# Optimization experiments

Hardware: AMD Instinct MI355X
Metric: run time of the kernel (lower is better)

## Reference

```python
import jax, jax.numpy as jnp
import numpy as np

EPSILON = 1e-13
LN_EPS = 1e-5
DIRECTIONS = 2
HID = 512


def setup_inputs() -> dict:
    key = jax.random.key(0)
    k1, k2, k3, k4 = jax.random.split(key, 4)
    B, N, D = 16, 1024, HID
    adj = jax.random.randint(k1, (B, N, N), 0, 3, dtype=jnp.int32)  # labels 0..2
    hid = jax.random.normal(k2, (B, N, D), dtype=jnp.float32)
    W = jax.random.normal(k3, (DIRECTIONS * D, D), dtype=jnp.float32) * (1.0 / np.sqrt(DIRECTIONS * D))
    b = jnp.zeros((D,), dtype=jnp.float32)
    gamma = jnp.ones((D,), dtype=jnp.float32)
    beta = jnp.zeros((D,), dtype=jnp.float32)
    return {"adj": adj, "hid": hid, "W": W, "b": b, "gamma": gamma, "beta": beta}


def _layer_norm(x, gamma, beta):
    mu = jnp.mean(x, axis=-1, keepdims=True)
    var = jnp.mean(jnp.square(x - mu), axis=-1, keepdims=True)
    return (x - mu) * jax.lax.rsqrt(var + LN_EPS) * gamma + beta


def reference(adj, hid, W, b, gamma, beta):
    residual = hid
    direct_list = []
    for j in range(DIRECTIONS):  # fixed small structural loop
        mask = (adj == (j + 1)).astype(hid.dtype)            # [B,N,N]
        weight = mask / (jnp.sum(mask, axis=-1, keepdims=True) + EPSILON)
        direct_list.append(jnp.einsum('bnm,bmd->bnd', weight, hid))
    out = jnp.concatenate(direct_list, axis=-1)              # [B,N,directions*D]
    out = out @ W + b                                        # [B,N,D]
    out = jax.nn.relu(out)
    out = out + residual
    return _layer_norm(out, gamma, beta)
```

## Files before the change

### kernel.cpp

```cpp
#include <hip/hip_runtime.h>

#define NB 16
#define NN 1024
#define ND 512

typedef __attribute__((ext_vector_type(8))) short short8;
typedef __attribute__((ext_vector_type(4))) float f32x4;

typedef const __attribute__((address_space(1))) void* gptr1;
typedef __attribute__((address_space(3))) void* lptr3;

#define VMCNT0() asm volatile("s_waitcnt vmcnt(0)" ::: "memory")
#define VMCNT1() asm volatile("s_waitcnt vmcnt(1)" ::: "memory")
#define LGKM0()  asm volatile("s_waitcnt lgkmcnt(0)" ::: "memory")
#define BAR()    __builtin_amdgcn_s_barrier()

static __device__ __forceinline__ unsigned f2bf(float f) {
  union { float f; unsigned u; } v; v.f = f;
  unsigned r = v.u + 0x7FFFu + ((v.u >> 16) & 1u);
  return r >> 16;
}

__global__ void k_wt(const float* __restrict__ W, unsigned short* __restrict__ WT) {
  __shared__ float t[64][65];
  int r0 = blockIdx.x * 64;
  int c0 = blockIdx.y * 64;
  int tid = threadIdx.x;
#pragma unroll
  for (int i = 0; i < 4; ++i) {
    int f = i * 256 + tid;
    int r = f >> 4, cq = f & 15;
    float4 v = *(const float4*)(W + (size_t)(r0 + r) * ND + c0 + cq * 4);
    t[r][cq * 4 + 0] = v.x; t[r][cq * 4 + 1] = v.y;
    t[r][cq * 4 + 2] = v.z; t[r][cq * 4 + 3] = v.w;
  }
  __syncthreads();
#pragma unroll
  for (int i = 0; i < 8; ++i) {
    int f = i * 256 + tid;
    int oc = f >> 5;
    int on = (f & 31) * 2;
    unsigned lo = f2bf(t[on][oc]), hi = f2bf(t[on + 1][oc]);
    *(unsigned*)(WT + (size_t)(c0 + oc) * NN + r0 + on) = lo | (hi << 16);
  }
}

__global__ void k_pack(const int* __restrict__ adj, unsigned* __restrict__ packed,
                       float* __restrict__ invc) {
  int wid = threadIdx.x >> 6, lane = threadIdx.x & 63;
  int wrow0 = (blockIdx.x * 4 + wid) * 4;
#pragma unroll
  for (int r = 0; r < 4; ++r) {
    int row = wrow0 + r;
    const int* p = adj + (size_t)row * NN + lane * 16;
    unsigned u = 0;
#pragma unroll
    for (int i = 0; i < 4; ++i) {
      int4 v = *(const int4*)(p + i * 4);
      u |= ((unsigned)v.x << (8 * i)) | ((unsigned)v.y << (8 * i + 2))
         | ((unsigned)v.z << (8 * i + 4)) | ((unsigned)v.w << (8 * i + 6));
    }
    packed[(size_t)row * 64 + lane] = u;
    unsigned c1 = __popc(u & 0x55555555u);
    unsigned c2 = __popc(u & 0xAAAAAAAAu);
    unsigned pr = c1 | (c2 << 16);
#pragma unroll
    for (int o = 32; o; o >>= 1) pr += __shfl_xor(pr, o);
    if (lane == 0) {
      invc[row * 2 + 0] = 1.0f / ((float)(pr & 0xFFFFu) + 1e-13f);
      invc[row * 2 + 1] = 1.0f / ((float)(pr >> 16) + 1e-13f);
    }
  }
}

__global__ __launch_bounds__(256, 2) void k_pre(
    const float* __restrict__ hid, const unsigned short* __restrict__ WT,
    unsigned short* __restrict__ Pt1, unsigned short* __restrict__ Pt2) {
  __shared__ __align__(16) char smem[49152];
  char* A1 = smem;
  char* A2 = smem + 16384;
  char* Bh = smem + 32768;

  int phys = blockIdx.x;
  int logical = (phys & 7) * 64 + (phys >> 3);
  int b = logical >> 5;
  int rem = logical & 31;
  int dt = rem >> 3, mt = rem & 7;
  int d0 = dt * 128, m0 = mt * 128;

  int tid = threadIdx.x, lane = tid & 63, wid = tid >> 6;
  int wr = wid >> 1, wc = wid & 1;

  const float* hb = hid + (size_t)b * NN * ND;

  f32x4 acc1[4][4], acc2[4][4];
  f32x4 zero = {0.f, 0.f, 0.f, 0.f};
#pragma unroll
  for (int i = 0; i < 4; ++i)
#pragma unroll
    for (int j = 0; j < 4; ++j) { acc1[i][j] = zero; acc2[i][j] = zero; }

  float4 fc[8], fn[8];
#pragma unroll
  for (int it = 0; it < 8; ++it) {
    int f = it * 256 + tid;
    fc[it] = *(const float4*)(hb + (size_t)(m0 + (f >> 4)) * ND + (f & 15) * 4);
  }
#pragma unroll
  for (int i = 0; i < 4; ++i) {
    int q = wid * 4 + i;
    int r = q * 8 + (lane >> 3);
    int sl = (lane & 7) ^ (r & 7);
    __builtin_amdgcn_global_load_lds((gptr1)(WT + (size_t)(d0 + r) * NN + sl * 8),
                                     (lptr3)(A1 + q * 1024), 16, 0, 0);
    __builtin_amdgcn_global_load_lds((gptr1)(WT + (size_t)(d0 + r) * NN + 512 + sl * 8),
                                     (lptr3)(A2 + q * 1024), 16, 0, 0);
  }

  for (int kt = 0; kt < 8; ++kt) {
    int k0 = kt * 64;
#pragma unroll
    for (int it = 0; it < 8; ++it) {
      int f = it * 256 + tid;
      int row = f >> 4, colq = f & 15;
      float4 v = fc[it];
      unsigned lo = f2bf(v.x) | (f2bf(v.y) << 16);
      unsigned hi = f2bf(v.z) | (f2bf(v.w) << 16);
      int addr = row * 128 + (((colq >> 1) ^ (row & 7)) * 16) + (colq & 1) * 8;
      *(uint2*)(Bh + addr) = make_uint2(lo, hi);
    }
    VMCNT0();
    if (kt < 7) {
#pragma unroll
      for (int it = 0; it < 8; ++it) {
        int f = it * 256 + tid;
        fn[it] = *(const float4*)(hb + (size_t)(m0 + (f >> 4)) * ND + k0 + 64 + (f & 15) * 4);
      }
    }
    LGKM0();
    BAR();
#pragma unroll
    for (int ks = 0; ks < 2; ++ks) {
      short8 a1[4], a2[4], bf[4];
#pragma unroll
      for (int mi = 0; mi < 4; ++mi) {
        int row = wr * 64 + mi * 16 + (lane & 15);
        int slot = (ks * 4 + (lane >> 4)) ^ (row & 7);
        a1[mi] = *(const short8*)(A1 + row * 128 + slot * 16);
        a2[mi] = *(const short8*)(A2 + row * 128 + slot * 16);
      }
#pragma unroll
      for (int nj = 0; nj < 4; ++nj) {
        int col = wc * 64 + nj * 16 + (lane & 15);
        int slot = (ks * 4 + (lane >> 4)) ^ (col & 7);
        bf[nj] = *(const short8*)(Bh + col * 128 + slot * 16);
      }
#pragma unroll
      for (int mi = 0; mi < 4; ++mi)
#pragma unroll
        for (int nj = 0; nj < 4; ++nj) {
          acc1[mi][nj] = __builtin_amdgcn_mfma_f32_16x16x32_bf16(a1[mi], bf[nj], acc1[mi][nj], 0, 0, 0);
          acc2[mi][nj] = __builtin_amdgcn_mfma_f32_16x16x32_bf16(a2[mi], bf[nj], acc2[mi][nj], 0, 0, 0);
        }
    }
    BAR();
    if (kt < 7) {
#pragma unroll
      for (int i = 0; i < 4; ++i) {
        int q = wid * 4 + i;
        int r = q * 8 + (lane >> 3);
        int sl = (lane & 7) ^ (r & 7);
        __builtin_amdgcn_global_load_lds((gptr1)(WT + (size_t)(d0 + r) * NN + k0 + 64 + sl * 8),
                                         (lptr3)(A1 + q * 1024), 16, 0, 0);
        __builtin_amdgcn_global_load_lds((gptr1)(WT + (size_t)(d0 + r) * NN + 512 + k0 + 64 + sl * 8),
                                         (lptr3)(A2 + q * 1024), 16, 0, 0);
      }
#pragma unroll
      for (int it = 0; it < 8; ++it) fc[it] = fn[it];
    }
    __builtin_amdgcn_sched_barrier(0);
  }
  unsigned short* P1b = Pt1 + (size_t)b * ND * NN;
  unsigned short* P2b = Pt2 + (size_t)b * ND * NN;
#pragma unroll
  for (int mi = 0; mi < 4; ++mi) {
#pragma unroll
    for (int rr = 0; rr < 4; ++rr) {
      int rowd = d0 + wr * 64 + mi * 16 + (lane >> 4) * 4 + rr;
#pragma unroll
      for (int nj = 0; nj < 4; ++nj) {
        int colm = m0 + wc * 64 + nj * 16 + (lane & 15);
        P1b[(size_t)rowd * NN + colm] = (unsigned short)f2bf(acc1[mi][nj][rr]);
        P2b[(size_t)rowd * NN + colm] = (unsigned short)f2bf(acc2[mi][nj][rr]);
      }
    }
  }
}

__global__ __launch_bounds__(256, 2) void k_main(
    const unsigned* __restrict__ packed, const unsigned short* __restrict__ Pt1,
    const unsigned short* __restrict__ Pt2, const float* __restrict__ invc,
    const float* __restrict__ bias, const float* __restrict__ hid,
    float* __restrict__ out) {
  __shared__ __align__(16) char smem[65536];
  char* A1 = smem;
  char* A2 = smem + 16384;
  char* B1 = smem + 32768;
  char* B2 = smem + 49152;

  int phys = blockIdx.x;
  int logical = (phys & 7) * 64 + (phys >> 3);
  int b = logical >> 5;
  int rem = logical & 31;
  int mt = rem >> 2, nt = rem & 3;
  int n0 = mt * 128, d0 = nt * 128;

  int tid = threadIdx.x, lane = tid & 63, wid = tid >> 6;
  int wr = wid >> 1, wc = wid & 1;
  int row = tid >> 1, half = tid & 1;

  const unsigned* pkb = packed + ((size_t)b * NN + n0 + row) * 64 + half * 2;
  const unsigned short* P1b = Pt1 + (size_t)b * ND * NN;
  const unsigned short* P2b = Pt2 + (size_t)b * ND * NN;

  f32x4 acc1[4][4], acc2[4][4];
  f32x4 zero = {0.f, 0.f, 0.f, 0.f};
#pragma unroll
  for (int i = 0; i < 4; ++i)
#pragma unroll
    for (int j = 0; j < 4; ++j) { acc1[i][j] = zero; acc2[i][j] = zero; }

  uint2 pc, pn;
  pc = *(const uint2*)pkb;
#pragma unroll
  for (int i = 0; i < 4; ++i) {
    int q = wid * 4 + i;
    int r = q * 8 + (lane >> 3);
    int sl = (lane & 7) ^ (r & 7);
    __builtin_amdgcn_global_load_lds((gptr1)(P1b + (size_t)(d0 + r) * NN + sl * 8),
                                     (lptr3)(B1 + q * 1024), 16, 0, 0);
    __builtin_amdgcn_global_load_lds((gptr1)(P2b + (size_t)(d0 + r) * NN + sl * 8),
                                     (lptr3)(B2 + q * 1024), 16, 0, 0);
  }
  __builtin_amdgcn_sched_barrier(0);

  for (int kt = 0; kt < 16; ++kt) {
    int k0 = kt * 64;
#pragma unroll
    for (int g = 0; g < 4; ++g) {
      unsigned w = (g < 2) ? pc.x : pc.y;
      unsigned bits = w >> ((g & 1) * 16);
      uint4 u1, u2;
      unsigned t0 = bits, t1 = bits >> 4, t2 = bits >> 8, t3 = bits >> 12;
      u1.x = (t0 & 1) * 0x3F80u | ((t0 >> 2) & 1) * 0x3F800000u;
      u2.x = ((t0 >> 1) & 1) * 0x3F80u | ((t0 >> 3) & 1) * 0x3F800000u;
      u1.y = (t1 & 1) * 0x3F80u | ((t1 >> 2) & 1) * 0x3F800000u;
      u2.y = ((t1 >> 1) & 1) * 0x3F80u | ((t1 >> 3) & 1) * 0x3F800000u;
      u1.z = (t2 & 1) * 0x3F80u | ((t2 >> 2) & 1) * 0x3F800000u;
      u2.z = ((t2 >> 1) & 1) * 0x3F80u | ((t2 >> 3) & 1) * 0x3F800000u;
      u1.w = (t3 & 1) * 0x3F80u | ((t3 >> 2) & 1) * 0x3F800000u;
      u2.w = ((t3 >> 1) & 1) * 0x3F80u | ((t3 >> 3) & 1) * 0x3F800000u;
      int slot = half * 4 + g;
      int addr = row * 128 + ((slot ^ (row & 7)) * 16);
      *(uint4*)(A1 + addr) = u1;
      *(uint4*)(A2 + addr) = u2;
    }
    if (kt < 15) {
      pn = *(const uint2*)(pkb + (kt + 1) * 4);
      VMCNT1();
    } else {
      VMCNT0();
    }
    LGKM0();
    BAR();
#pragma unroll
    for (int ks = 0; ks < 2; ++ks) {
      short8 a1[4], a2[4], b1[4], b2[4];
#pragma unroll
      for (int mi = 0; mi < 4; ++mi) {
        int r = wr * 64 + mi * 16 + (lane & 15);
        int slot = (ks * 4 + (lane >> 4)) ^ (r & 7);
        a1[mi] = *(const short8*)(A1 + r * 128 + slot * 16);
        a2[mi] = *(const short8*)(A2 + r * 128 + slot * 16);
      }
#pragma unroll
      for (int nj = 0; nj < 4; ++nj) {
        int c = wc * 64 + nj * 16 + (lane & 15);
        int slot = (ks * 4 + (lane >> 4)) ^ (c & 7);
        b1[nj] = *(const short8*)(B1 + c * 128 + slot * 16);
        b2[nj] = *(const short8*)(B2 + c * 128 + slot * 16);
      }
#pragma unroll
      for (int mi = 0; mi < 4; ++mi)
#pragma unroll
        for (int nj = 0; nj < 4; ++nj) {
          acc1[mi][nj] = __builtin_amdgcn_mfma_f32_16x16x32_bf16(a1[mi], b1[nj], acc1[mi][nj], 0, 0, 0);
          acc2[mi][nj] = __builtin_amdgcn_mfma_f32_16x16x32_bf16(a2[mi], b2[nj], acc2[mi][nj], 0, 0, 0);
        }
    }
    BAR();
    if (kt < 15) {
#pragma unroll
      for (int i = 0; i < 4; ++i) {
        int q = wid * 4 + i;
        int r = q * 8 + (lane >> 3);
        int sl = (lane & 7) ^ (r & 7);
        __builtin_amdgcn_global_load_lds((gptr1)(P1b + (size_t)(d0 + r) * NN + k0 + 64 + sl * 8),
                                         (lptr3)(B1 + q * 1024), 16, 0, 0);
        __builtin_amdgcn_global_load_lds((gptr1)(P2b + (size_t)(d0 + r) * NN + k0 + 64 + sl * 8),
                                         (lptr3)(B2 + q * 1024), 16, 0, 0);
      }
      pc = pn;
    }
    __builtin_amdgcn_sched_barrier(0);
  }
#pragma unroll
  for (int mi = 0; mi < 4; ++mi) {
#pragma unroll
    for (int rr = 0; rr < 4; ++rr) {
      int n = n0 + wr * 64 + mi * 16 + (lane >> 4) * 4 + rr;
      float i1 = invc[((size_t)b * NN + n) * 2 + 0];
      float i2 = invc[((size_t)b * NN + n) * 2 + 1];
      const float* hrow = hid + ((size_t)b * NN + n) * ND;
      float* orow = out + ((size_t)b * NN + n) * ND;
#pragma unroll
      for (int nj = 0; nj < 4; ++nj) {
        int d = d0 + wc * 64 + nj * 16 + (lane & 15);
        float v = acc1[mi][nj][rr] * i1 + acc2[mi][nj][rr] * i2 + bias[d];
        v = fmaxf(v, 0.f);
        orow[d] = v + hrow[d];
      }
    }
  }
}

__global__ void k_ln(float* __restrict__ out, const float* __restrict__ gamma,
                     const float* __restrict__ beta) {
  int row = blockIdx.x * 4 + (threadIdx.x >> 6);
  int lane = threadIdx.x & 63;
  float* p = out + (size_t)row * ND;
  float4 x0 = *(const float4*)(p + lane * 4);
  float4 x1 = *(const float4*)(p + 256 + lane * 4);
  float s = x0.x + x0.y + x0.z + x0.w + x1.x + x1.y + x1.z + x1.w;
#pragma unroll
  for (int o = 32; o; o >>= 1) s += __shfl_xor(s, o);
  float mu = s * (1.0f / 512.0f);
  float d0x = x0.x - mu, d0y = x0.y - mu, d0z = x0.z - mu, d0w = x0.w - mu;
  float d1x = x1.x - mu, d1y = x1.y - mu, d1z = x1.z - mu, d1w = x1.w - mu;
  float v = d0x * d0x + d0y * d0y + d0z * d0z + d0w * d0w
          + d1x * d1x + d1y * d1y + d1z * d1z + d1w * d1w;
#pragma unroll
  for (int o = 32; o; o >>= 1) v += __shfl_xor(v, o);
  float rs = rsqrtf(v * (1.0f / 512.0f) + 1e-5f);
  float4 g0 = *(const float4*)(gamma + lane * 4);
  float4 g1 = *(const float4*)(gamma + 256 + lane * 4);
  float4 b0 = *(const float4*)(beta + lane * 4);
  float4 b1 = *(const float4*)(beta + 256 + lane * 4);
  float4 y0, y1;
  y0.x = d0x * rs * g0.x + b0.x; y0.y = d0y * rs * g0.y + b0.y;
  y0.z = d0z * rs * g0.z + b0.z; y0.w = d0w * rs * g0.w + b0.w;
  y1.x = d1x * rs * g1.x + b1.x; y1.y = d1y * rs * g1.y + b1.y;
  y1.z = d1z * rs * g1.z + b1.z; y1.w = d1w * rs * g1.w + b1.w;
  *(float4*)(p + lane * 4) = y0;
  *(float4*)(p + 256 + lane * 4) = y1;
}

extern "C" void kernel_launch(void* const* d_in, const int* in_sizes, int n_in,
                              void* d_out, int out_size, void* d_ws, size_t ws_size,
                              hipStream_t stream) {
  (void)in_sizes; (void)n_in; (void)out_size; (void)ws_size;
  const int*   adj   = (const int*)d_in[0];
  const float* hid   = (const float*)d_in[1];
  const float* W     = (const float*)d_in[2];
  const float* bias  = (const float*)d_in[3];
  const float* gamma = (const float*)d_in[4];
  const float* beta  = (const float*)d_in[5];
  float* out = (float*)d_out;

  char* ws = (char*)d_ws;
  unsigned short* WT     = (unsigned short*)ws;
  unsigned short* Pt1    = (unsigned short*)(ws + 1048576);
  unsigned short* Pt2    = (unsigned short*)(ws + 17825792);
  unsigned*       packed = (unsigned*)(ws + 34603008);
  float*          invc   = (float*)(ws + 38797312);

  k_wt  <<<dim3(16, 8), 256, 0, stream>>>(W, WT);
  k_pack<<<1024, 256, 0, stream>>>(adj, packed, invc);
  k_pre <<<512, 256, 0, stream>>>(hid, WT, Pt1, Pt2);
  k_main<<<512, 256, 0, stream>>>(packed, Pt1, Pt2, invc, bias, hid, out);
  k_ln  <<<4096, 256, 0, stream>>>(out, gamma, beta);
}
```

Baseline: 99.45 us.

## Drop LDS staging in main GEMM and pass bf16 pre-norm output to LayerNorm

The main aggregation GEMM stops staging A and B tiles through shared memory with barriers. Each lane now loads its B fragments straight from global memory into registers, prefetching the next k-step, and builds its A fragments from packed adjacency bits in registers. The pre-LayerNorm intermediate is stored as bf16 in a workspace buffer instead of fp32 in the output, which halves that write and the LayerNorm read. The trade-off is more redundant global B loads across waves, higher register pressure, and lower precision in the LayerNorm input.

```diff
diff --git a/kernel.cpp b/kernel.cpp
--- a/kernel.cpp
+++ b/kernel.cpp
@@ -11,14 +11,19 @@
 typedef __attribute__((address_space(3))) void* lptr3;
 
 #define VMCNT0() asm volatile("s_waitcnt vmcnt(0)" ::: "memory")
-#define VMCNT1() asm volatile("s_waitcnt vmcnt(1)" ::: "memory")
 #define LGKM0()  asm volatile("s_waitcnt lgkmcnt(0)" ::: "memory")
 #define BAR()    __builtin_amdgcn_s_barrier()
+
+union U8 { uint4 u; short8 s; };
 
 static __device__ __forceinline__ unsigned f2bf(float f) {
   union { float f; unsigned u; } v; v.f = f;
   unsigned r = v.u + 0x7FFFu + ((v.u >> 16) & 1u);
   return r >> 16;
+}
+static __device__ __forceinline__ float bf2f(unsigned short h) {
+  union { unsigned u; float f; } v; v.u = ((unsigned)h) << 16;
+  return v.f;
 }
 
 __global__ void k_wt(const float* __restrict__ W, unsigned short* __restrict__ WT) {
@@ -201,13 +206,7 @@
     const unsigned* __restrict__ packed, const unsigned short* __restrict__ Pt1,
     const unsigned short* __restrict__ Pt2, const float* __restrict__ invc,
     const float* __restrict__ bias, const float* __restrict__ hid,
-    float* __restrict__ out) {
-  __shared__ __align__(16) char smem[65536];
-  char* A1 = smem;
-  char* A2 = smem + 16384;
-  char* B1 = smem + 32768;
-  char* B2 = smem + 49152;
-
+    unsigned short* __restrict__ preS) {
   int phys = blockIdx.x;
   int logical = (phys & 7) * 64 + (phys >> 3);
   int b = logical >> 5;
@@ -217,11 +216,16 @@
 
   int tid = threadIdx.x, lane = tid & 63, wid = tid >> 6;
   int wr = wid >> 1, wc = wid & 1;
-  int row = tid >> 1, half = tid & 1;
-
-  const unsigned* pkb = packed + ((size_t)b * NN + n0 + row) * 64 + half * 2;
-  const unsigned short* P1b = Pt1 + (size_t)b * ND * NN;
-  const unsigned short* P2b = Pt2 + (size_t)b * ND * NN;
+  int l15 = lane & 15, lq = lane >> 4;
+  unsigned sh = (lq & 1) << 4;
+
+  const unsigned* cp[4];
+#pragma unroll
+  for (int mi = 0; mi < 4; ++mi)
+    cp[mi] = packed + ((size_t)b * NN + n0 + wr * 64 + mi * 16 + l15) * 64 + (lq >> 1);
+
+  const unsigned short* bp1 = Pt1 + ((size_t)b * ND + d0 + wc * 64 + l15) * NN + lq * 8;
+  const unsigned short* bp2 = Pt2 + ((size_t)b * ND + d0 + wc * 64 + l15) * NN + lq * 8;
 
   f32x4 acc1[4][4], acc2[4][4];
   f32x4 zero = {0.f, 0.f, 0.f, 0.f};
@@ -230,139 +234,131 @@
 #pragma unroll
     for (int j = 0; j < 4; ++j) { acc1[i][j] = zero; acc2[i][j] = zero; }
 
-  uint2 pc, pn;
-  pc = *(const uint2*)pkb;
-#pragma unroll
-  for (int i = 0; i < 4; ++i) {
-    int q = wid * 4 + i;
-    int r = q * 8 + (lane >> 3);
-    int sl = (lane & 7) ^ (r & 7);
-    __builtin_amdgcn_global_load_lds((gptr1)(P1b + (size_t)(d0 + r) * NN + sl * 8),
-                                     (lptr3)(B1 + q * 1024), 16, 0, 0);
-    __builtin_amdgcn_global_load_lds((gptr1)(P2b + (size_t)(d0 + r) * NN + sl * 8),
-                                     (lptr3)(B2 + q * 1024), 16, 0, 0);
-  }
-  __builtin_amdgcn_sched_barrier(0);
-
+  unsigned creg[4][2];
+  short8 breg[2][2][4];
+#pragma unroll
+  for (int mi = 0; mi < 4; ++mi) {
+    creg[mi][0] = cp[mi][0];
+    creg[mi][1] = cp[mi][2];
+  }
+#pragma unroll
+  for (int ks = 0; ks < 2; ++ks)
+#pragma unroll
+    for (int nj = 0; nj < 4; ++nj) {
+      breg[0][ks][nj] = *(const short8*)(bp1 + nj * 16 * NN + ks * 32);
+      breg[1][ks][nj] = *(const short8*)(bp2 + nj * 16 * NN + ks * 32);
+    }
+
+#pragma unroll 1
   for (int kt = 0; kt < 16; ++kt) {
-    int k0 = kt * 64;
-#pragma unroll
-    for (int g = 0; g < 4; ++g) {
-      unsigned w = (g < 2) ? pc.x : pc.y;
-      unsigned bits = w >> ((g & 1) * 16);
-      uint4 u1, u2;
-      unsigned t0 = bits, t1 = bits >> 4, t2 = bits >> 8, t3 = bits >> 12;
-      u1.x = (t0 & 1) * 0x3F80u | ((t0 >> 2) & 1) * 0x3F800000u;
-      u2.x = ((t0 >> 1) & 1) * 0x3F80u | ((t0 >> 3) & 1) * 0x3F800000u;
-      u1.y = (t1 & 1) * 0x3F80u | ((t1 >> 2) & 1) * 0x3F800000u;
-      u2.y = ((t1 >> 1) & 1) * 0x3F80u | ((t1 >> 3) & 1) * 0x3F800000u;
-      u1.z = (t2 & 1) * 0x3F80u | ((t2 >> 2) & 1) * 0x3F800000u;
-      u2.z = ((t2 >> 1) & 1) * 0x3F80u | ((t2 >> 3) & 1) * 0x3F800000u;
-      u1.w = (t3 & 1) * 0x3F80u | ((t3 >> 2) & 1) * 0x3F800000u;
-      u2.w = ((t3 >> 1) & 1) * 0x3F80u | ((t3 >> 3) & 1) * 0x3F800000u;
-      int slot = half * 4 + g;
-      int addr = row * 128 + ((slot ^ (row & 7)) * 16);
-      *(uint4*)(A1 + addr) = u1;
-      *(uint4*)(A2 + addr) = u2;
-    }
-    if (kt < 15) {
-      pn = *(const uint2*)(pkb + (kt + 1) * 4);
-      VMCNT1();
-    } else {
-      VMCNT0();
-    }
-    LGKM0();
-    BAR();
-#pragma unroll
-    for (int ks = 0; ks < 2; ++ks) {
-      short8 a1[4], a2[4], b1[4], b2[4];
-#pragma unroll
-      for (int mi = 0; mi < 4; ++mi) {
-        int r = wr * 64 + mi * 16 + (lane & 15);
-        int slot = (ks * 4 + (lane >> 4)) ^ (r & 7);
-        a1[mi] = *(const short8*)(A1 + r * 128 + slot * 16);
-        a2[mi] = *(const short8*)(A2 + r * 128 + slot * 16);
-      }
-#pragma unroll
-      for (int nj = 0; nj < 4; ++nj) {
-        int c = wc * 64 + nj * 16 + (lane & 15);
-        int slot = (ks * 4 + (lane >> 4)) ^ (c & 7);
-        b1[nj] = *(const short8*)(B1 + c * 128 + slot * 16);
-        b2[nj] = *(const short8*)(B2 + c * 128 + slot * 16);
-      }
-#pragma unroll
-      for (int mi = 0; mi < 4; ++mi)
-#pragma unroll
-        for (int nj = 0; nj < 4; ++nj) {
-          acc1[mi][nj] = __builtin_amdgcn_mfma_f32_16x16x32_bf16(a1[mi], b1[nj], acc1[mi][nj], 0, 0, 0);
-          acc2[mi][nj] = __builtin_amdgcn_mfma_f32_16x16x32_bf16(a2[mi], b2[nj], acc2[mi][nj], 0, 0, 0);
-        }
-    }
-    BAR();
-    if (kt < 15) {
-#pragma unroll
-      for (int i = 0; i < 4; ++i) {
-        int q = wid * 4 + i;
-        int r = q * 8 + (lane >> 3);
-        int sl = (lane & 7) ^ (r & 7);
-        __builtin_amdgcn_global_load_lds((gptr1)(P1b + (size_t)(d0 + r) * NN + k0 + 64 + sl * 8),
-                                         (lptr3)(B1 + q * 1024), 16, 0, 0);
-        __builtin_amdgcn_global_load_lds((gptr1)(P2b + (size_t)(d0 + r) * NN + k0 + 64 + sl * 8),
-                                         (lptr3)(B2 + q * 1024), 16, 0, 0);
-      }
-      pc = pn;
-    }
-    __builtin_amdgcn_sched_barrier(0);
-  }
+    U8 a1[4], a2[4];
+#pragma unroll
+    for (int mi = 0; mi < 4; ++mi) {
+      unsigned h = creg[mi][0] >> sh;
+#pragma unroll
+      for (int j = 0; j < 4; ++j) {
+        unsigned t1 = (h >> (4 * j)) & 5u;
+        a1[mi].u[j] = ((t1 | (t1 << 14)) & 0x00010001u) * 0x3F80u;
+        unsigned t2 = (h >> (4 * j + 1)) & 5u;
+        a2[mi].u[j] = ((t2 | (t2 << 14)) & 0x00010001u) * 0x3F80u;
+      }
+    }
+#pragma unroll
+    for (int nj = 0; nj < 4; ++nj) {
+#pragma unroll
+      for (int mi = 0; mi < 4; ++mi)
+        acc1[mi][nj] = __builtin_amdgcn_mfma_f32_16x16x32_bf16(a1[mi].s, breg[0][0][nj], acc1[mi][nj], 0, 0, 0);
+#pragma unroll
+      for (int mi = 0; mi < 4; ++mi)
+        acc2[mi][nj] = __builtin_amdgcn_mfma_f32_16x16x32_bf16(a2[mi].s, breg[1][0][nj], acc2[mi][nj], 0, 0, 0);
+      breg[0][0][nj] = *(const short8*)(bp1 + nj * 16 * NN + 64);
+      breg[1][0][nj] = *(const short8*)(bp2 + nj * 16 * NN + 64);
+    }
+#pragma unroll
+    for (int mi = 0; mi < 4; ++mi) {
+      unsigned h = creg[mi][1] >> sh;
+#pragma unroll
+      for (int j = 0; j < 4; ++j) {
+        unsigned t1 = (h >> (4 * j)) & 5u;
+        a1[mi].u[j] = ((t1 | (t1 << 14)) & 0x00010001u) * 0x3F80u;
+        unsigned t2 = (h >> (4 * j + 1)) & 5u;
+        a2[mi].u[j] = ((t2 | (t2 << 14)) & 0x00010001u) * 0x3F80u;
+      }
+    }
+#pragma unroll
+    for (int mi = 0; mi < 4; ++mi) {
+      creg[mi][0] = cp[mi][4];
+      creg[mi][1] = cp[mi][6];
+    }
+#pragma unroll
+    for (int nj = 0; nj < 4; ++nj) {
+#pragma unroll
+      for (int mi = 0; mi < 4; ++mi)
+        acc1[mi][nj] = __builtin_amdgcn_mfma_f32_16x16x32_bf16(a1[mi].s, breg[0][1][nj], acc1[mi][nj], 0, 0, 0);
+#pragma unroll
+      for (int mi = 0; mi < 4; ++mi)
+        acc2[mi][nj] = __builtin_amdgcn_mfma_f32_16x16x32_bf16(a2[mi].s, breg[1][1][nj], acc2[mi][nj], 0, 0, 0);
+      breg[0][1][nj] = *(const short8*)(bp1 + nj * 16 * NN + 32 + 64);
+      breg[1][1][nj] = *(const short8*)(bp2 + nj * 16 * NN + 32 + 64);
+    }
+#pragma unroll
+    for (int mi = 0; mi < 4; ++mi) cp[mi] += 4;
+    bp1 += 64; bp2 += 64;
+  }
+
 #pragma unroll
   for (int mi = 0; mi < 4; ++mi) {
 #pragma unroll
     for (int rr = 0; rr < 4; ++rr) {
-      int n = n0 + wr * 64 + mi * 16 + (lane >> 4) * 4 + rr;
+      int n = n0 + wr * 64 + mi * 16 + lq * 4 + rr;
       float i1 = invc[((size_t)b * NN + n) * 2 + 0];
       float i2 = invc[((size_t)b * NN + n) * 2 + 1];
       const float* hrow = hid + ((size_t)b * NN + n) * ND;
-      float* orow = out + ((size_t)b * NN + n) * ND;
+      unsigned short* prow = preS + ((size_t)b * NN + n) * ND;
 #pragma unroll
       for (int nj = 0; nj < 4; ++nj) {
-        int d = d0 + wc * 64 + nj * 16 + (lane & 15);
+        int d = d0 + wc * 64 + nj * 16 + l15;
         float v = acc1[mi][nj][rr] * i1 + acc2[mi][nj][rr] * i2 + bias[d];
         v = fmaxf(v, 0.f);
-        orow[d] = v + hrow[d];
-      }
-    }
-  }
-}
-
-__global__ void k_ln(float* __restrict__ out, const float* __restrict__ gamma,
-                     const float* __restrict__ beta) {
+        v += hrow[d];
+        prow[d] = (unsigned short)f2bf(v);
+      }
+    }
+  }
+}
+
+__global__ void k_ln(const unsigned short* __restrict__ preS, float* __restrict__ out,
+                     const float* __restrict__ gamma, const float* __restrict__ beta) {
   int row = blockIdx.x * 4 + (threadIdx.x >> 6);
   int lane = threadIdx.x & 63;
-  float* p = out + (size_t)row * ND;
-  float4 x0 = *(const float4*)(p + lane * 4);
-  float4 x1 = *(const float4*)(p + 256 + lane * 4);
-  float s = x0.x + x0.y + x0.z + x0.w + x1.x + x1.y + x1.z + x1.w;
+  short8 raw = *(const short8*)(preS + (size_t)row * ND + lane * 8);
+  float x[8];
+#pragma unroll
+  for (int i = 0; i < 8; ++i) x[i] = bf2f((unsigned short)raw[i]);
+  float s = 0.f;
+#pragma unroll
+  for (int i = 0; i < 8; ++i) s += x[i];
 #pragma unroll
   for (int o = 32; o; o >>= 1) s += __shfl_xor(s, o);
   float mu = s * (1.0f / 512.0f);
-  float d0x = x0.x - mu, d0y = x0.y - mu, d0z = x0.z - mu, d0w = x0.w - mu;
-  float d1x = x1.x - mu, d1y = x1.y - mu, d1z = x1.z - mu, d1w = x1.w - mu;
-  float v = d0x * d0x + d0y * d0y + d0z * d0z + d0w * d0w
-          + d1x * d1x + d1y * d1y + d1z * d1z + d1w * d1w;
+  float v = 0.f;
+#pragma unroll
+  for (int i = 0; i < 8; ++i) { float d = x[i] - mu; v += d * d; }
 #pragma unroll
   for (int o = 32; o; o >>= 1) v += __shfl_xor(v, o);
   float rs = rsqrtf(v * (1.0f / 512.0f) + 1e-5f);
-  float4 g0 = *(const float4*)(gamma + lane * 4);
-  float4 g1 = *(const float4*)(gamma + 256 + lane * 4);
-  float4 b0 = *(const float4*)(beta + lane * 4);
-  float4 b1 = *(const float4*)(beta + 256 + lane * 4);
+  float4 g0 = *(const float4*)(gamma + lane * 8);
+  float4 g1 = *(const float4*)(gamma + lane * 8 + 4);
+  float4 b0 = *(const float4*)(beta + lane * 8);
+  float4 b1 = *(const float4*)(beta + lane * 8 + 4);
   float4 y0, y1;
-  y0.x = d0x * rs * g0.x + b0.x; y0.y = d0y * rs * g0.y + b0.y;
-  y0.z = d0z * rs * g0.z + b0.z; y0.w = d0w * rs * g0.w + b0.w;
-  y1.x = d1x * rs * g1.x + b1.x; y1.y = d1y * rs * g1.y + b1.y;
-  y1.z = d1z * rs * g1.z + b1.z; y1.w = d1w * rs * g1.w + b1.w;
-  *(float4*)(p + lane * 4) = y0;
-  *(float4*)(p + 256 + lane * 4) = y1;
+  y0.x = (x[0] - mu) * rs * g0.x + b0.x; y0.y = (x[1] - mu) * rs * g0.y + b0.y;
+  y0.z = (x[2] - mu) * rs * g0.z + b0.z; y0.w = (x[3] - mu) * rs * g0.w + b0.w;
+  y1.x = (x[4] - mu) * rs * g1.x + b1.x; y1.y = (x[5] - mu) * rs * g1.y + b1.y;
+  y1.z = (x[6] - mu) * rs * g1.z + b1.z; y1.w = (x[7] - mu) * rs * g1.w + b1.w;
+  float* p = out + (size_t)row * ND + lane * 8;
+  *(float4*)p = y0;
+  *(float4*)(p + 4) = y1;
 }
 
 extern "C" void kernel_launch(void* const* d_in, const int* in_sizes, int n_in,
@@ -383,10 +379,11 @@
   unsigned short* Pt2    = (unsigned short*)(ws + 17825792);
   unsigned*       packed = (unsigned*)(ws + 34603008);
   float*          invc   = (float*)(ws + 38797312);
+  unsigned short* preS   = (unsigned short*)(ws + 38928384);
 
   k_wt  <<<dim3(16, 8), 256, 0, stream>>>(W, WT);
   k_pack<<<1024, 256, 0, stream>>>(adj, packed, invc);
   k_pre <<<512, 256, 0, stream>>>(hid, WT, Pt1, Pt2);
-  k_main<<<512, 256, 0, stream>>>(packed, Pt1, Pt2, invc, bias, hid, out);
-  k_ln  <<<4096, 256, 0, stream>>>(out, gamma, beta);
-}
+  k_main<<<512, 256, 0, stream>>>(packed, Pt1, Pt2, invc, bias, hid, preS);
+  k_ln  <<<4096, 256, 0, stream>>>(preS, out, gamma, beta);
+}
```

After: 147.2 us. 1.48x slower.
